# Performance work log

Hardware: AMD Instinct MI355X
Metric: run time of the kernel (lower is better)

Reference implementation:

```python
import jax, jax.numpy as jnp
import numpy as np

NUM_PATCHES = 16
QPB = 20          # qubits per tree block
NBLOCKS = 4
N = 1 << QPB      # 2**20 amplitudes per block statevector
INV_SQRT2 = 0.7071067811865476


def _single_qubit_states(x, pos_weights):
    """H @ (data-encoding rotations) |0> for every wire, grouped into blocks.
    x: (B,16,4,3) color angles; pos_weights: (16,2). Returns (B,4,20,2) c64.
    The leading Hadamard of the layer-1 IQP unitary is folded in here since
    the pre-layer-1 state is a tensor product of single-qubit states."""
    B = x.shape[0]
    hx, hy, hz = 0.5 * x[..., 0], 0.5 * x[..., 1], 0.5 * x[..., 2]
    v0 = jnp.cos(hx) + 0j
    v1 = -1j * jnp.sin(hx)                       # RX|0>
    cy, sy = jnp.cos(hy), jnp.sin(hy)
    w0 = cy * v0 - sy * v1
    w1 = sy * v0 + cy * v1                       # RY
    pz = jnp.exp(-1j * hz)
    w0 = pz * w0
    w1 = jnp.conj(pz) * w1                       # RZ
    color = jnp.stack([w0 + w1, w0 - w1], -1) * INV_SQRT2       # H  -> (B,16,4,2)

    px, py = 0.5 * pos_weights[:, 0], 0.5 * pos_weights[:, 1]
    a0 = jnp.cos(px) + 0j
    a1 = -1j * jnp.sin(px)                       # RX|0>
    cy, sy = jnp.cos(py), jnp.sin(py)
    b0 = cy * a0 - sy * a1
    b1 = sy * a0 + cy * a1                       # RY
    anc = jnp.stack([b0 + b1, b0 - b1], -1) * INV_SQRT2         # (16,2)
    anc = jnp.broadcast_to(anc[None, :, None, :], (B, NUM_PATCHES, 1, 2))

    states = jnp.concatenate([color, anc], axis=2)              # (B,16,5,2)
    return states.reshape(B, NBLOCKS, QPB, 2).astype(jnp.complex64)


def _forward(x, pos_weights, layer_1_weights, layer_2_weights, head_w, head_b):
    B = x.shape[0]
    states = _single_qubit_states(x, pos_weights)   # (B,4,20,2)

    # Build each block's 2^20 product statevector (wire 0 = slowest index).
    psi = states[:, :, 0, :]
    for q in range(1, QPB):
        psi = (psi[..., None] * states[:, :, q][:, :, None, :]).reshape(B, NBLOCKS, -1)

    # Layer-1 diagonal: RZ(a_i) + ring IsingZZ(b_i); phase exp(-i/2 (a.z + b.(z*roll(z)))).
    idx = jnp.arange(N, dtype=jnp.uint32)
    shifts = (QPB - 1 - jnp.arange(QPB, dtype=jnp.uint32))
    z = 1.0 - 2.0 * ((idx[None, :] >> shifts[:, None]) & 1).astype(jnp.float32)  # (20,N)
    a1, b1 = layer_1_weights[:, 0], layer_1_weights[:, 1]
    theta = a1 @ z + b1 @ (z * jnp.roll(z, -1, axis=0))
    psi = psi * jnp.exp(-0.5j * theta).astype(jnp.complex64)

    # Closing Hadamard layer of layer-1 IQP = Walsh-Hadamard transform on 20 wires.
    for i in range(QPB):
        psi = psi.reshape(B, NBLOCKS, 1 << i, 2, 1 << (QPB - 1 - i))
        p0, p1 = psi[:, :, :, 0, :], psi[:, :, :, 1, :]
        psi = jnp.stack([p0 + p1, p0 - p1], axis=3) * INV_SQRT2
    psi = psi.reshape(B, NBLOCKS, N)

    # Reduced density matrix on the 4 surviving qubits (first 4 wires) of each block.
    A = psi.reshape(B, NBLOCKS, 16, N // 16)
    rho4 = jnp.einsum('bkim,bkjm->bkij', A, jnp.conj(A))        # (B,4,16,16)
    r = rho4.reshape(B, NBLOCKS, 2, 2, 2, 2, 2, 2, 2, 2)
    rho012 = jnp.einsum('bkpqrxstux->bkpqrstu', r).reshape(B, NBLOCKS, 8, 8)
    rho123 = jnp.einsum('bkxpqrxstu->bkpqrstu', r).reshape(B, NBLOCKS, 8, 8)
    rho01  = jnp.einsum('bkpqxystxy->bkpqst', r).reshape(B, NBLOCKS, 4, 4)
    rho23  = jnp.einsum('bkxypqxyst->bkpqst', r).reshape(B, NBLOCKS, 4, 4)
    rho_q0 = jnp.einsum('bkpxyzqxyz->bkpq', r)                  # (B,4,2,2)
    rho_q3 = jnp.einsum('bkxyzpxyzq->bkpq', r)

    # Layer-2 IQP (H D H) in Heisenberg picture: U2^dag Z_k U2 =
    #   Z_k exp(-i a_k X_k) exp(-i b_{k-1} X_{k-1} X_k) exp(-i b_k X_k X_{k+1}),
    # a 3-qubit operator on ring positions (k-1, k, k+1) of the 16 survivors.
    I2 = jnp.eye(2, dtype=jnp.complex64)
    X = jnp.array([[0, 1], [1, 0]], dtype=jnp.complex64)
    Z = jnp.array([[1, 0], [0, -1]], dtype=jnp.complex64)
    I8 = jnp.eye(8, dtype=jnp.complex64)
    IZI = jnp.kron(I2, jnp.kron(Z, I2))
    IXI = jnp.kron(I2, jnp.kron(X, I2))
    XXI = jnp.kron(X, jnp.kron(X, I2))
    IXX = jnp.kron(I2, jnp.kron(X, X))

    def rot(t, P):
        return jnp.cos(t) * I8 - 1j * jnp.sin(t) * P

    a2, b2 = layer_2_weights[:, 0], layer_2_weights[:, 1]

    def heis_op(k):
        return IZI @ rot(a2[k], IXI) @ rot(b2[(k - 1) % 16], XXI) @ rot(b2[k], IXX)

    def tr(O, rho):  # Re Tr[O rho] per batch element
        return jnp.real(jnp.einsum('ij,bji->b', O, rho))

    # Blocks are independent before layer 2 -> cross-block joints are tensor products.
    # Ring position 15 = block 3 survivor q3; position 4 = block 1 survivor q0.
    rho_k0 = jnp.einsum('bij,bkl->bikjl', rho_q3[:, 3], rho01[:, 0]).reshape(B, 8, 8)
    rho_k3 = jnp.einsum('bij,bkl->bikjl', rho23[:, 0], rho_q0[:, 1]).reshape(B, 8, 8)

    e0 = tr(heis_op(0), rho_k0)
    e1 = tr(heis_op(1), rho012[:, 0])
    e2 = tr(heis_op(2), rho123[:, 0])
    e3 = tr(heis_op(3), rho_k3)
    q_out = jnp.stack([e0, e1, e2, e3], axis=-1).astype(jnp.float32)  # (B,4)

    out = q_out @ head_w.T + head_b
    norm = jnp.linalg.norm(out, axis=-1, keepdims=True)
    return out / jnp.maximum(norm, 1e-12)


def setup_inputs() -> dict:
    key = jax.random.key(0)
    ks = jax.random.split(key, 6)
    B = 8
    x = jax.random.uniform(ks[0], (B, NUM_PATCHES, 4, 3), dtype=jnp.float32,
                           minval=0.0, maxval=np.pi)
    pos_weights = jax.random.normal(ks[1], (16, 2), dtype=jnp.float32) * 0.01
    layer_1_weights = jax.random.normal(ks[2], (20, 2), dtype=jnp.float32) * 0.1
    layer_2_weights = jax.random.normal(ks[3], (16, 2), dtype=jnp.float32) * 0.1
    head_w = jax.random.normal(ks[4], (512, 4), dtype=jnp.float32) * 0.1
    head_b = jax.random.normal(ks[5], (512,), dtype=jnp.float32) * 0.01
    return {'x': x, 'pos_weights': pos_weights, 'layer_1_weights': layer_1_weights,
            'layer_2_weights': layer_2_weights, 'head_w': head_w, 'head_b': head_b}


def reference(x, pos_weights, layer_1_weights, layer_2_weights, head_w, head_b):
    return _forward(x, pos_weights, layer_1_weights, layer_2_weights, head_w, head_b)
```

## Files before the change

kernel.cpp:

```cpp
#include <hip/hip_runtime.h>
#include <math.h>

#define INV_SQRT2F 0.70710678118654752f

__device__ __forceinline__ float2 cmul(float2 a, float2 b) {
  return make_float2(a.x*b.x - a.y*b.y, a.x*b.y + a.y*b.x);
}
__device__ __forceinline__ float2 cmulc(float2 a, float2 b) {
  return make_float2(a.x*b.x + a.y*b.y, a.y*b.x - a.x*b.y);
}
__device__ __forceinline__ float2 cadd(float2 a, float2 b) {
  return make_float2(a.x + b.x, a.y + b.y);
}

__global__ __launch_bounds__(1024) void iqp_fused_kernel(
    const float* __restrict__ x,
    const float* __restrict__ pw,
    const float* __restrict__ lw,
    const float* __restrict__ l2,
    const float* __restrict__ hw,
    const float* __restrict__ hb,
    float* __restrict__ out)
{
  const int b = blockIdx.x;
  const int t = threadIdx.x;
  const int lane = t & 63;

  __shared__ float2 sqs[4][20][2];
  __shared__ float  b1s[20];
  __shared__ float2 W[4][4][8][33];
  __shared__ float2 D[4][8][64];
  __shared__ float2 rho[4][256];
  __shared__ float2 r012[64], r123[64], rk0[64], rk3[64];
  __shared__ float2 r01[16], r23[16], q0s[4], q3s[4];
  __shared__ float  e[4];
  __shared__ float  wsum[8];
  __shared__ float  nrm;

  if (t < 80) {
    const int k2 = t / 20, q = t % 20;
    const int pch = 4*k2 + q/5;
    const int j = q % 5;
    float2 s0, s1;
    if (j < 4) {
      const float* xp = x + ((size_t)((b*16 + pch)*4 + j))*3;
      const float hx = 0.5f*xp[0], hy = 0.5f*xp[1], hz = 0.5f*xp[2];
      const float cx = cosf(hx), sx = sinf(hx);
      const float cy = cosf(hy), sy = sinf(hy);
      const float cz = cosf(hz), sz = sinf(hz);
      float2 w0 = make_float2(cy*cx,  sy*sx);
      float2 w1 = make_float2(sy*cx, -cy*sx);
      w0 = cmul(make_float2(cz, -sz), w0);
      w1 = cmul(make_float2(cz,  sz), w1);
      s0 = make_float2((w0.x + w1.x)*INV_SQRT2F, (w0.y + w1.y)*INV_SQRT2F);
      s1 = make_float2((w0.x - w1.x)*INV_SQRT2F, (w0.y - w1.y)*INV_SQRT2F);
    } else {
      const float px = 0.5f*pw[2*pch], py = 0.5f*pw[2*pch + 1];
      const float cx = cosf(px), sx = sinf(px);
      const float cy = cosf(py), sy = sinf(py);
      const float2 w0 = make_float2(cy*cx,  sy*sx);
      const float2 w1 = make_float2(sy*cx, -cy*sx);
      s0 = make_float2((w0.x + w1.x)*INV_SQRT2F, (w0.y + w1.y)*INV_SQRT2F);
      s1 = make_float2((w0.x - w1.x)*INV_SQRT2F, (w0.y - w1.y)*INV_SQRT2F);
    }
    const float ha = 0.5f*lw[2*q];
    const float ca = cosf(ha), sa = sinf(ha);
    sqs[k2][q][0] = cmul(s0, make_float2(ca, -sa));
    sqs[k2][q][1] = cmul(s1, make_float2(ca,  sa));
    if (k2 == 0) b1s[q] = lw[2*q + 1];
  }
  __syncthreads();

  const int kk = t >> 8;
  const int cls = (t >> 6) & 3;

  {
    const int b0 = cls & 1, b9 = cls >> 1;
    float2 v[4];
    #pragma unroll
    for (int j = 0; j < 4; ++j) {
      const int m = j*64 + lane;
      const int r = (b0 << 9) | (m << 1) | b9;
      float2 prod = make_float2(1.f, 0.f);
      int bits[10];
      #pragma unroll
      for (int q = 0; q < 10; ++q) {
        bits[q] = (r >> (9 - q)) & 1;
        prod = cmul(prod, sqs[kk][q][bits[q]]);
      }
      float phi = 0.f;
      #pragma unroll
      for (int q = 0; q < 9; ++q) {
        const float zq  = 1.f - 2.f*(float)bits[q];
        const float zq1 = 1.f - 2.f*(float)bits[q + 1];
        phi += b1s[q]*zq*zq1;
      }
      const float hp = 0.5f*phi;
      v[j] = cmul(prod, make_float2(cosf(hp), -sinf(hp)));
    }
    {
      float2 a0 = v[0], a2 = v[2];
      v[0] = cadd(a0, a2); v[2] = make_float2(a0.x - a2.x, a0.y - a2.y);
      float2 a1 = v[1], a3 = v[3];
      v[1] = cadd(a1, a3); v[3] = make_float2(a1.x - a3.x, a1.y - a3.y);
      a0 = v[0]; a1 = v[1];
      v[0] = cadd(a0, a1); v[1] = make_float2(a0.x - a1.x, a0.y - a1.y);
      a2 = v[2]; a3 = v[3];
      v[2] = cadd(a2, a3); v[3] = make_float2(a2.x - a3.x, a2.y - a3.y);
    }
    #pragma unroll
    for (int mask = 1; mask <= 32; mask <<= 1) {
      #pragma unroll
      for (int j = 0; j < 4; ++j) {
        const float px = __shfl_xor(v[j].x, mask);
        const float py = __shfl_xor(v[j].y, mask);
        if (lane & mask) v[j] = make_float2(px - v[j].x, py - v[j].y);
        else             v[j] = make_float2(v[j].x + px, v[j].y + py);
      }
    }
    #pragma unroll
    for (int j = 0; j < 4; ++j) {
      const int m = j*64 + lane;
      W[kk][cls][m >> 5][m & 31] =
          make_float2(v[j].x*0.0625f, v[j].y*0.0625f);
    }
  }
  __syncthreads();

  #pragma unroll
  for (int rep = 0; rep < 2; ++rep) {
    const int o = t + rep*1024;
    const int dk = o >> 9, rem = o & 511;
    const int pr = rem >> 6, xx = (rem >> 3) & 7, yy = rem & 7;
    const int pa = pr >> 1;
    const int pb = (pr & 1) + ((pr >> 2) << 1);
    float2 acc = make_float2(0.f, 0.f);
    #pragma unroll 8
    for (int u = 0; u < 32; ++u)
      acc = cadd(acc, cmulc(W[dk][pa][xx][u], W[dk][pb][yy][u]));
    D[dk][pr][xx*8 + yy] = acc;
  }
  __syncthreads();

  {
    const int dk = t >> 8, ij = t & 255;
    const int i = ij >> 4, j = ij & 15;
    const int xy = (i & 7)*8 + (j & 7);
    const int si = i >> 3, sj = j >> 3;
    const float2 q19a = sqs[dk][19][0], q19b = sqs[dk][19][1];
    const float s19a = q19a.x*q19a.x + q19a.y*q19a.y;
    const float s19b = q19b.x*q19b.x + q19b.y*q19b.y;
    const float b119 = b1s[19];
    const float cb = cosf(b119), sb = sinf(b119);
    const float2 gam = make_float2((s19a + s19b)*cb, (s19b - s19a)*sb);
    float2 acc = cadd(D[dk][0][xy], D[dk][4][xy]);
    {
      const float2 t2 = cadd(D[dk][3][xy], D[dk][7][xy]);
      const float sg = ((si ^ sj) & 1) ? -1.f : 1.f;
      acc.x += sg*t2.x; acc.y += sg*t2.y;
    }
    {
      float2 t3 = cadd(D[dk][1][xy], D[dk][5][xy]);
      t3 = cmul(gam, t3);
      const float sg = (sj & 1) ? -1.f : 1.f;
      acc.x += sg*t3.x; acc.y += sg*t3.y;
    }
    {
      float2 t4 = cadd(D[dk][2][xy], D[dk][6][xy]);
      t4 = cmulc(t4, gam);
      const float sg = (si & 1) ? -1.f : 1.f;
      acc.x += sg*t4.x; acc.y += sg*t4.y;
    }
    rho[dk][ij] = make_float2(0.5f*acc.x, 0.5f*acc.y);
  }
  __syncthreads();

  if (t < 64) {
    const int i = t >> 3, j = t & 7;
    r012[t] = cadd(rho[0][(2*i)*16 + 2*j], rho[0][(2*i + 1)*16 + 2*j + 1]);
    r123[t] = cadd(rho[0][i*16 + j], rho[0][(i + 8)*16 + (j + 8)]);
  }
  if (t < 16) {
    const int i = t >> 2, j = t & 3;
    float2 s1 = make_float2(0.f, 0.f), s2 = make_float2(0.f, 0.f);
    for (int w = 0; w < 4; ++w) {
      s1 = cadd(s1, rho[0][(4*i + w)*16 + 4*j + w]);
      s2 = cadd(s2, rho[0][(4*w + i)*16 + 4*w + j]);
    }
    r01[t] = s1;  r23[t] = s2;
  }
  if (t < 4) {
    const int i = t >> 1, j = t & 1;
    float2 s1 = make_float2(0.f, 0.f), s2 = make_float2(0.f, 0.f);
    for (int w = 0; w < 8; ++w) {
      s1 = cadd(s1, rho[1][(8*i + w)*16 + 8*j + w]);
      s2 = cadd(s2, rho[3][(2*w + i)*16 + 2*w + j]);
    }
    q0s[t] = s1;  q3s[t] = s2;
  }
  __syncthreads();

  if (t < 64) {
    const int i = t >> 3, j = t & 7;
    rk0[t] = cmul(q3s[(i >> 2)*2 + (j >> 2)], r01[(i & 3)*4 + (j & 3)]);
    rk3[t] = cmul(r23[(i >> 1)*4 + (j >> 1)], q0s[(i & 1)*2 + (j & 1)]);
  }
  __syncthreads();

  if (t < 256) {
    const int k = t >> 6;
    const int idx = t & 63;
    const int i = idx >> 3, j = idx & 7;
    const float alpha = l2[2*k];
    const float beta1 = l2[2*((k + 15) & 15) + 1];
    const float beta2 = l2[2*k + 1];
    const float ca = cosf(alpha), sa = sinf(alpha);
    const float cb1 = cosf(beta1), sb1 = sinf(beta1);
    const float cb2 = cosf(beta2), sb2 = sinf(beta2);
    float2 m1, m2;
    {
      const int xr = i ^ j;
      m1 = (xr == 0) ? make_float2( cb1*cb2, 0.f)
         : (xr == 3) ? make_float2( 0.f,    -cb1*sb2)
         : (xr == 6) ? make_float2( 0.f,    -sb1*cb2)
         : (xr == 5) ? make_float2(-sb1*sb2, 0.f)
         : make_float2(0.f, 0.f);
      const int xr2 = xr ^ 2;
      m2 = (xr2 == 0) ? make_float2( cb1*cb2, 0.f)
         : (xr2 == 3) ? make_float2( 0.f,    -cb1*sb2)
         : (xr2 == 6) ? make_float2( 0.f,    -sb1*cb2)
         : (xr2 == 5) ? make_float2(-sb1*sb2, 0.f)
         : make_float2(0.f, 0.f);
    }
    float2 O = make_float2(ca*m1.x + sa*m2.y, ca*m1.y - sa*m2.x);
    if ((i >> 1) & 1) { O.x = -O.x; O.y = -O.y; }
    const float2* rp = (k == 0) ? rk0 : (k == 1) ? r012 : (k == 2) ? r123 : rk3;
    const float2 rv = rp[j*8 + i];
    float contrib = O.x*rv.x - O.y*rv.y;
    for (int off = 32; off > 0; off >>= 1) contrib += __shfl_down(contrib, off);
    if (idx == 0) e[k] = contrib;
  }
  __syncthreads();

  float val = 0.f;
  if (t < 512) {
    val = hb[t] + e[0]*hw[4*t] + e[1]*hw[4*t + 1]
        + e[2]*hw[4*t + 2] + e[3]*hw[4*t + 3];
    float ss = val*val;
    for (int off = 32; off > 0; off >>= 1) ss += __shfl_down(ss, off);
    if ((t & 63) == 0) wsum[t >> 6] = ss;
  }
  __syncthreads();
  if (t == 0) {
    float s = 0.f;
    for (int w = 0; w < 8; ++w) s += wsum[w];
    nrm = fmaxf(sqrtf(s), 1e-12f);
  }
  __syncthreads();
  if (t < 512) out[(size_t)b*512 + t] = val / nrm;
}

extern "C" void kernel_launch(void* const* d_in, const int* in_sizes, int n_in,
                              void* d_out, int out_size, void* d_ws, size_t ws_size,
                              hipStream_t stream) {
  const float* x  = (const float*)d_in[0];
  const float* pw = (const float*)d_in[1];
  const float* lw = (const float*)d_in[2];
  const float* l2 = (const float*)d_in[3];
  const float* hw = (const float*)d_in[4];
  const float* hb = (const float*)d_in[5];
  const int B = in_sizes[0] / (16*4*3);

  iqp_fused_kernel<<<B, 1024, 0, stream>>>(x, pw, lw, l2, hw, hb, (float*)d_out);
}
```

Measured before the change: 76.16 us.

## Skip unused block-2 density matrix, compute only needed reduced traces, use fast sincos

The kernel now processes only blocks 0, 1 and 3 and drops block 2, whose reduced density matrix was never used. For block 1 it skips the Walsh-Hadamard transform and computes only the six inner products needed for the single-qubit marginal q0s. For block 3 it computes the 2x2 marginal directly with per-warp partial sums, instead of building the full D and rho matrices. All transcendental calls switch to __sincosf/__cosf, which cuts special-function cost but lowers accuracy slightly.

```diff
diff --git a/kernel.cpp b/kernel.cpp
--- a/kernel.cpp
+++ b/kernel.cpp
@@ -25,29 +25,33 @@
   const int b = blockIdx.x;
   const int t = threadIdx.x;
   const int lane = t & 63;
-
-  __shared__ float2 sqs[4][20][2];
+  const int wid = t >> 6;
+
+  __shared__ float2 sqs[3][20][2];
   __shared__ float  b1s[20];
-  __shared__ float2 W[4][4][8][33];
-  __shared__ float2 D[4][8][64];
-  __shared__ float2 rho[4][256];
+  __shared__ float2 W[3][4][8][33];
+  __shared__ float2 D0[8][64];
+  __shared__ float2 ipv[6];
+  __shared__ float2 q3part[4][3];
+  __shared__ float2 rho[256];
   __shared__ float2 r012[64], r123[64], rk0[64], rk3[64];
   __shared__ float2 r01[16], r23[16], q0s[4], q3s[4];
   __shared__ float  e[4];
   __shared__ float  wsum[8];
   __shared__ float  nrm;
 
-  if (t < 80) {
-    const int k2 = t / 20, q = t % 20;
-    const int pch = 4*k2 + q/5;
+  if (t < 60) {
+    const int kidx = t / 20, q = t % 20;
+    const int k = (kidx == 2) ? 3 : kidx;
+    const int pch = 4*k + q/5;
     const int j = q % 5;
     float2 s0, s1;
     if (j < 4) {
       const float* xp = x + ((size_t)((b*16 + pch)*4 + j))*3;
-      const float hx = 0.5f*xp[0], hy = 0.5f*xp[1], hz = 0.5f*xp[2];
-      const float cx = cosf(hx), sx = sinf(hx);
-      const float cy = cosf(hy), sy = sinf(hy);
-      const float cz = cosf(hz), sz = sinf(hz);
+      float cx, sx, cy, sy, cz, sz;
+      __sincosf(0.5f*xp[0], &sx, &cx);
+      __sincosf(0.5f*xp[1], &sy, &cy);
+      __sincosf(0.5f*xp[2], &sz, &cz);
       float2 w0 = make_float2(cy*cx,  sy*sx);
       float2 w1 = make_float2(sy*cx, -cy*sx);
       w0 = cmul(make_float2(cz, -sz), w0);
@@ -55,26 +59,25 @@
       s0 = make_float2((w0.x + w1.x)*INV_SQRT2F, (w0.y + w1.y)*INV_SQRT2F);
       s1 = make_float2((w0.x - w1.x)*INV_SQRT2F, (w0.y - w1.y)*INV_SQRT2F);
     } else {
-      const float px = 0.5f*pw[2*pch], py = 0.5f*pw[2*pch + 1];
-      const float cx = cosf(px), sx = sinf(px);
-      const float cy = cosf(py), sy = sinf(py);
+      float cx, sx, cy, sy;
+      __sincosf(0.5f*pw[2*pch], &sx, &cx);
+      __sincosf(0.5f*pw[2*pch + 1], &sy, &cy);
       const float2 w0 = make_float2(cy*cx,  sy*sx);
       const float2 w1 = make_float2(sy*cx, -cy*sx);
       s0 = make_float2((w0.x + w1.x)*INV_SQRT2F, (w0.y + w1.y)*INV_SQRT2F);
       s1 = make_float2((w0.x - w1.x)*INV_SQRT2F, (w0.y - w1.y)*INV_SQRT2F);
     }
-    const float ha = 0.5f*lw[2*q];
-    const float ca = cosf(ha), sa = sinf(ha);
-    sqs[k2][q][0] = cmul(s0, make_float2(ca, -sa));
-    sqs[k2][q][1] = cmul(s1, make_float2(ca,  sa));
-    if (k2 == 0) b1s[q] = lw[2*q + 1];
-  }
-  __syncthreads();
-
-  const int kk = t >> 8;
-  const int cls = (t >> 6) & 3;
-
-  {
+    float ca, sa;
+    __sincosf(0.5f*lw[2*q], &sa, &ca);
+    sqs[kidx][q][0] = cmul(s0, make_float2(ca, -sa));
+    sqs[kidx][q][1] = cmul(s1, make_float2(ca,  sa));
+    if (kidx == 0) b1s[q] = lw[2*q + 1];
+  }
+  __syncthreads();
+
+  if (wid < 12) {
+    const int kk = wid >> 2;
+    const int cls = wid & 3;
     const int b0 = cls & 1, b9 = cls >> 1;
     float2 v[4];
     #pragma unroll
@@ -95,108 +98,170 @@
         const float zq1 = 1.f - 2.f*(float)bits[q + 1];
         phi += b1s[q]*zq*zq1;
       }
-      const float hp = 0.5f*phi;
-      v[j] = cmul(prod, make_float2(cosf(hp), -sinf(hp)));
-    }
-    {
-      float2 a0 = v[0], a2 = v[2];
-      v[0] = cadd(a0, a2); v[2] = make_float2(a0.x - a2.x, a0.y - a2.y);
-      float2 a1 = v[1], a3 = v[3];
-      v[1] = cadd(a1, a3); v[3] = make_float2(a1.x - a3.x, a1.y - a3.y);
-      a0 = v[0]; a1 = v[1];
-      v[0] = cadd(a0, a1); v[1] = make_float2(a0.x - a1.x, a0.y - a1.y);
-      a2 = v[2]; a3 = v[3];
-      v[2] = cadd(a2, a3); v[3] = make_float2(a2.x - a3.x, a2.y - a3.y);
-    }
-    #pragma unroll
-    for (int mask = 1; mask <= 32; mask <<= 1) {
+      float sp, cp;
+      __sincosf(0.5f*phi, &sp, &cp);
+      v[j] = cmul(prod, make_float2(cp, -sp));
+    }
+    if (kk != 1) {
+      {
+        float2 a0 = v[0], a2 = v[2];
+        v[0] = cadd(a0, a2); v[2] = make_float2(a0.x - a2.x, a0.y - a2.y);
+        float2 a1 = v[1], a3 = v[3];
+        v[1] = cadd(a1, a3); v[3] = make_float2(a1.x - a3.x, a1.y - a3.y);
+        a0 = v[0]; a1 = v[1];
+        v[0] = cadd(a0, a1); v[1] = make_float2(a0.x - a1.x, a0.y - a1.y);
+        a2 = v[2]; a3 = v[3];
+        v[2] = cadd(a2, a3); v[3] = make_float2(a2.x - a3.x, a2.y - a3.y);
+      }
       #pragma unroll
-      for (int j = 0; j < 4; ++j) {
-        const float px = __shfl_xor(v[j].x, mask);
-        const float py = __shfl_xor(v[j].y, mask);
-        if (lane & mask) v[j] = make_float2(px - v[j].x, py - v[j].y);
-        else             v[j] = make_float2(v[j].x + px, v[j].y + py);
-      }
-    }
+      for (int mask = 1; mask <= 32; mask <<= 1) {
+        #pragma unroll
+        for (int j = 0; j < 4; ++j) {
+          const float px = __shfl_xor(v[j].x, mask);
+          const float py = __shfl_xor(v[j].y, mask);
+          if (lane & mask) v[j] = make_float2(px - v[j].x, py - v[j].y);
+          else             v[j] = make_float2(v[j].x + px, v[j].y + py);
+        }
+      }
+    }
+    const float scl = (kk == 1) ? 1.0f : 0.0625f;
     #pragma unroll
     for (int j = 0; j < 4; ++j) {
       const int m = j*64 + lane;
       W[kk][cls][m >> 5][m & 31] =
-          make_float2(v[j].x*0.0625f, v[j].y*0.0625f);
-    }
-  }
-  __syncthreads();
-
-  #pragma unroll
-  for (int rep = 0; rep < 2; ++rep) {
-    const int o = t + rep*1024;
-    const int dk = o >> 9, rem = o & 511;
-    const int pr = rem >> 6, xx = (rem >> 3) & 7, yy = rem & 7;
+          make_float2(v[j].x*scl, v[j].y*scl);
+    }
+  }
+  __syncthreads();
+
+  if (wid < 8) {
+    const int pr = t >> 6, idx = t & 63, xx = idx >> 3, yy = idx & 7;
     const int pa = pr >> 1;
     const int pb = (pr & 1) + ((pr >> 2) << 1);
     float2 acc = make_float2(0.f, 0.f);
     #pragma unroll 8
     for (int u = 0; u < 32; ++u)
-      acc = cadd(acc, cmulc(W[dk][pa][xx][u], W[dk][pb][yy][u]));
-    D[dk][pr][xx*8 + yy] = acc;
-  }
-  __syncthreads();
-
-  {
-    const int dk = t >> 8, ij = t & 255;
-    const int i = ij >> 4, j = ij & 15;
+      acc = cadd(acc, cmulc(W[0][pa][xx][u], W[0][pb][yy][u]));
+    D0[pr][xx*8 + yy] = acc;
+  } else if (wid < 12) {
+    const int w4 = wid - 8;
+    const int prl[6][2] = {{0,0},{1,1},{2,2},{3,3},{0,1},{2,3}};
+    #pragma unroll
+    for (int rep = 0; rep < 2; ++rep) {
+      const int which = (rep == 0) ? w4 : w4 + 4;
+      if (rep == 1 && w4 >= 2) break;
+      const int pa = prl[which][0], pb = prl[which][1];
+      float2 acc = make_float2(0.f, 0.f);
+      #pragma unroll
+      for (int jj = 0; jj < 4; ++jj) {
+        const int m = jj*64 + lane;
+        acc = cadd(acc, cmulc(W[1][pa][m >> 5][m & 31],
+                              W[1][pb][m >> 5][m & 31]));
+      }
+      for (int off = 32; off > 0; off >>= 1) {
+        acc.x += __shfl_down(acc.x, off);
+        acc.y += __shfl_down(acc.y, off);
+      }
+      if (lane == 0) ipv[which] = acc;
+    }
+  } else {
+    const int c = wid - 12;
+    const int lo = lane >> 4;
+    const int u0 = (lane & 15)*2;
+    float2 a00 = make_float2(0.f, 0.f), a01 = a00, a11 = a00;
+    #pragma unroll
+    for (int du = 0; du < 2; ++du) {
+      const float2 p0 = W[2][c][(lo << 1)    ][u0 + du];
+      const float2 p1 = W[2][c][(lo << 1) | 1][u0 + du];
+      a00 = cadd(a00, cmulc(p0, p0));
+      a01 = cadd(a01, cmulc(p0, p1));
+      a11 = cadd(a11, cmulc(p1, p1));
+    }
+    for (int off = 32; off > 0; off >>= 1) {
+      a00.x += __shfl_down(a00.x, off); a00.y += __shfl_down(a00.y, off);
+      a01.x += __shfl_down(a01.x, off); a01.y += __shfl_down(a01.y, off);
+      a11.x += __shfl_down(a11.x, off); a11.y += __shfl_down(a11.y, off);
+    }
+    if (lane == 0) {
+      q3part[c][0] = a00; q3part[c][1] = a01; q3part[c][2] = a11;
+    }
+  }
+  __syncthreads();
+
+  if (t < 256) {
+    const int i = t >> 4, j = t & 15;
     const int xy = (i & 7)*8 + (j & 7);
     const int si = i >> 3, sj = j >> 3;
-    const float2 q19a = sqs[dk][19][0], q19b = sqs[dk][19][1];
+    const float2 q19a = sqs[0][19][0], q19b = sqs[0][19][1];
     const float s19a = q19a.x*q19a.x + q19a.y*q19a.y;
     const float s19b = q19b.x*q19b.x + q19b.y*q19b.y;
-    const float b119 = b1s[19];
-    const float cb = cosf(b119), sb = sinf(b119);
+    const float cb = __cosf(b1s[19]), sb = __sinf(b1s[19]);
     const float2 gam = make_float2((s19a + s19b)*cb, (s19b - s19a)*sb);
-    float2 acc = cadd(D[dk][0][xy], D[dk][4][xy]);
+    float2 acc = cadd(D0[0][xy], D0[4][xy]);
     {
-      const float2 t2 = cadd(D[dk][3][xy], D[dk][7][xy]);
+      const float2 t2 = cadd(D0[3][xy], D0[7][xy]);
       const float sg = ((si ^ sj) & 1) ? -1.f : 1.f;
       acc.x += sg*t2.x; acc.y += sg*t2.y;
     }
     {
-      float2 t3 = cadd(D[dk][1][xy], D[dk][5][xy]);
+      float2 t3 = cadd(D0[1][xy], D0[5][xy]);
       t3 = cmul(gam, t3);
       const float sg = (sj & 1) ? -1.f : 1.f;
       acc.x += sg*t3.x; acc.y += sg*t3.y;
     }
     {
-      float2 t4 = cadd(D[dk][2][xy], D[dk][6][xy]);
+      float2 t4 = cadd(D0[2][xy], D0[6][xy]);
       t4 = cmulc(t4, gam);
       const float sg = (si & 1) ? -1.f : 1.f;
       acc.x += sg*t4.x; acc.y += sg*t4.y;
     }
-    rho[dk][ij] = make_float2(0.5f*acc.x, 0.5f*acc.y);
+    rho[t] = make_float2(0.5f*acc.x, 0.5f*acc.y);
+  } else if (t < 260) {
+    const int pp = (t - 256) >> 1, qq = (t - 256) & 1;
+    const float2 q19a = sqs[1][19][0], q19b = sqs[1][19][1];
+    const float s19a = q19a.x*q19a.x + q19a.y*q19a.y;
+    const float s19b = q19b.x*q19b.x + q19b.y*q19b.y;
+    const float cb = __cosf(b1s[19]), sb = __sinf(b1s[19]);
+    const float2 gam1 = make_float2((s19a + s19b)*cb, (s19b - s19a)*sb);
+    const float2 T04 = cadd(ipv[0], ipv[2]);
+    const float2 T37 = cadd(ipv[1], ipv[3]);
+    const float2 T15 = cadd(ipv[4], ipv[5]);
+    const float2 h = cmul(gam1, T15);
+    float2 acc = T04;
+    const float sg1 = ((pp ^ qq) & 1) ? -1.f : 1.f;
+    acc.x += sg1*T37.x; acc.y += sg1*T37.y;
+    const float sgq = (qq & 1) ? -1.f : 1.f;
+    acc.x += sgq*h.x; acc.y += sgq*h.y;
+    const float sgp = (pp & 1) ? -1.f : 1.f;
+    acc.x += sgp*h.x; acc.y -= sgp*h.y;
+    q0s[pp*2 + qq] = make_float2(0.5f*acc.x, 0.5f*acc.y);
+  } else if (t < 264) {
+    const int ei = t - 260;
+    const int pp = ei >> 1, qq = ei & 1;
+    const int src = (pp == 0 && qq == 0) ? 0 : (pp == 1 && qq == 1) ? 2 : 1;
+    float2 s = make_float2(0.f, 0.f);
+    #pragma unroll
+    for (int c = 0; c < 4; ++c) s = cadd(s, q3part[c][src]);
+    if (pp == 1 && qq == 0) s.y = -s.y;
+    q3s[pp*2 + qq] = s;
   }
   __syncthreads();
 
   if (t < 64) {
     const int i = t >> 3, j = t & 7;
-    r012[t] = cadd(rho[0][(2*i)*16 + 2*j], rho[0][(2*i + 1)*16 + 2*j + 1]);
-    r123[t] = cadd(rho[0][i*16 + j], rho[0][(i + 8)*16 + (j + 8)]);
-  }
-  if (t < 16) {
-    const int i = t >> 2, j = t & 3;
+    r012[t] = cadd(rho[(2*i)*16 + 2*j], rho[(2*i + 1)*16 + 2*j + 1]);
+    r123[t] = cadd(rho[i*16 + j], rho[(i + 8)*16 + (j + 8)]);
+  }
+  if (t >= 64 && t < 80) {
+    const int tt = t - 64;
+    const int i = tt >> 2, j = tt & 3;
     float2 s1 = make_float2(0.f, 0.f), s2 = make_float2(0.f, 0.f);
+    #pragma unroll
     for (int w = 0; w < 4; ++w) {
-      s1 = cadd(s1, rho[0][(4*i + w)*16 + 4*j + w]);
-      s2 = cadd(s2, rho[0][(4*w + i)*16 + 4*w + j]);
-    }
-    r01[t] = s1;  r23[t] = s2;
-  }
-  if (t < 4) {
-    const int i = t >> 1, j = t & 1;
-    float2 s1 = make_float2(0.f, 0.f), s2 = make_float2(0.f, 0.f);
-    for (int w = 0; w < 8; ++w) {
-      s1 = cadd(s1, rho[1][(8*i + w)*16 + 8*j + w]);
-      s2 = cadd(s2, rho[3][(2*w + i)*16 + 2*w + j]);
-    }
-    q0s[t] = s1;  q3s[t] = s2;
+      s1 = cadd(s1, rho[(4*i + w)*16 + 4*j + w]);
+      s2 = cadd(s2, rho[(4*w + i)*16 + 4*w + j]);
+    }
+    r01[tt] = s1;  r23[tt] = s2;
   }
   __syncthreads();
 
@@ -214,9 +279,10 @@
     const float alpha = l2[2*k];
     const float beta1 = l2[2*((k + 15) & 15) + 1];
     const float beta2 = l2[2*k + 1];
-    const float ca = cosf(alpha), sa = sinf(alpha);
-    const float cb1 = cosf(beta1), sb1 = sinf(beta1);
-    const float cb2 = cosf(beta2), sb2 = sinf(beta2);
+    float ca, sa, cb1, sb1, cb2, sb2;
+    __sincosf(alpha, &sa, &ca);
+    __sincosf(beta1, &sb1, &cb1);
+    __sincosf(beta2, &sb2, &cb2);
     float2 m1, m2;
     {
       const int xr = i ^ j;
```

After: 69.96 us. -8.1%, faster.
